# Performance work log

Hardware: AMD Instinct MI355X
Metric: run time of the kernel (lower is better)

Reference implementation:

```python
import jax, jax.numpy as jnp
import numpy as np

N = 50000
E = 600000
D_IN = 128
D_HID = 128
D_OUT = 128


def _glorot(key, shape):
    fan_in, fan_out = shape[0], shape[1]
    lim = float(np.sqrt(6.0 / (fan_in + fan_out)))
    return jax.random.uniform(key, shape, jnp.float32, -lim, lim)


def setup_inputs() -> dict:
    key = jax.random.key(0)
    ks = jax.random.split(key, 10)
    x = jax.random.normal(ks[0], (N, D_IN), jnp.float32)
    edge_index = jax.random.randint(ks[1], (2, E), 0, N, jnp.int64)
    # layer 1 params
    W_pool1 = _glorot(ks[2], (D_IN, D_HID))
    b_pool1 = jnp.zeros((D_HID,), jnp.float32)
    W_upd1 = _glorot(ks[3], (D_IN + D_HID, D_HID))
    b_upd1 = jnp.zeros((D_HID,), jnp.float32)
    # layer 2 params
    W_pool2 = _glorot(ks[4], (D_HID, D_OUT))
    b_pool2 = jnp.zeros((D_OUT,), jnp.float32)
    W_upd2 = _glorot(ks[5], (D_HID + D_OUT, D_OUT))
    b_upd2 = jnp.zeros((D_OUT,), jnp.float32)
    return {
        "x": x, "edge_index": edge_index,
        "W_pool1": W_pool1, "b_pool1": b_pool1, "W_upd1": W_upd1, "b_upd1": b_upd1,
        "W_pool2": W_pool2, "b_pool2": b_pool2, "W_upd2": W_upd2, "b_upd2": b_upd2,
    }


def _pool_sage_conv(x, src, dst, W_pool, b_pool, W_upd, b_upd):
    # message: ReLU(W_pool x_j + b) on gathered source features  [E, out]
    msg = jax.nn.relu(x[src] @ W_pool + b_pool)
    # aggregate: element-wise max over incoming edges per destination node
    agg = jax.ops.segment_max(msg, dst, num_segments=x.shape[0])
    # nodes with no in-edges get -inf from segment_max; torch code zeros non-finite
    agg = jnp.where(jnp.isfinite(agg), agg, jnp.zeros_like(agg))
    # update: ReLU(W_upd [x_v ; h_N(v)] + b)
    out = jax.nn.relu(jnp.concatenate([x, agg], axis=-1) @ W_upd + b_upd)
    return out


def reference(x, edge_index,
              W_pool1, b_pool1, W_upd1, b_upd1,
              W_pool2, b_pool2, W_upd2, b_upd2):
    src, dst = edge_index[0], edge_index[1]
    h = _pool_sage_conv(x, src, dst, W_pool1, b_pool1, W_upd1, b_upd1)
    h = _pool_sage_conv(h, src, dst, W_pool2, b_pool2, W_upd2, b_upd2)
    return h
```

## Files before the change

kernel.cpp:

```cpp
#include <hip/hip_runtime.h>

#define D 128
#define SLOTS 64
#define SLOTP 66
#define NBUCK 800
#define BSLOT 1024
#define EPB 8192

typedef __attribute__((ext_vector_type(8))) short bf16x8;
typedef __attribute__((ext_vector_type(4))) float f32x4;
typedef __attribute__((ext_vector_type(8))) unsigned short u16x8;

__device__ __forceinline__ unsigned short f2bf(float f) {
    unsigned u = __float_as_uint(f);
    u = u + 0x7fffu + ((u >> 16) & 1u);
    return (unsigned short)(u >> 16);
}

__device__ __forceinline__ void pack_one(const float* __restrict__ W,
                                         unsigned short* __restrict__ out, int g, int l) {
    const int kt = g >> 3, nt = g & 7;
    u16x8 pv;
#pragma unroll
    for (int j = 0; j < 8; ++j)
        pv[j] = f2bf(W[(size_t)(kt * 32 + (l >> 4) * 8 + j) * D + nt * 16 + (l & 15)]);
    *(u16x8*)&out[((size_t)g * 64 + l) * 8] = pv;
}

__global__ void prep_kernel(const float4* __restrict__ x4, ushort4* __restrict__ xb4, int n4,
                            const float* __restrict__ Wp1, const float* __restrict__ Wu1,
                            const float* __restrict__ Wp2, const float* __restrict__ Wu2,
                            unsigned short* __restrict__ Wp1p, unsigned short* __restrict__ Wu1p,
                            unsigned short* __restrict__ Wp2p, unsigned short* __restrict__ Wu2p,
                            const int* __restrict__ src, const int* __restrict__ dst,
                            int* __restrict__ gcur, int* __restrict__ bebuf, int E,
                            int EB1, int CB) {
    int b = blockIdx.x;
    const int t = threadIdx.x;
    if (b < EB1) {
        __shared__ int hist[NBUCK];
        __shared__ int boff[NBUCK];
        for (int i = t; i < NBUCK; i += 256) hist[i] = 0;
        __syncthreads();
        const int4* dst4 = (const int4*)dst;
        const int4* src4 = (const int4*)src;
        const int q0 = b * (EPB / 4);
        const int nq = (E + 3) / 4;
#pragma unroll
        for (int k = 0; k < EPB / 4; k += 256) {
            int qi = q0 + k + t;
            if (qi < nq) {
                int4 d4 = dst4[qi];
                int e = qi * 4;
                if (e + 0 < E) atomicAdd(&hist[d4.x >> 6], 1);
                if (e + 1 < E) atomicAdd(&hist[d4.y >> 6], 1);
                if (e + 2 < E) atomicAdd(&hist[d4.z >> 6], 1);
                if (e + 3 < E) atomicAdd(&hist[d4.w >> 6], 1);
            }
        }
        __syncthreads();
        for (int i = t; i < NBUCK; i += 256) {
            int c = hist[i];
            boff[i] = c ? atomicAdd(&gcur[i], c) : 0;
            hist[i] = 0;
        }
        __syncthreads();
#pragma unroll
        for (int k = 0; k < EPB / 4; k += 256) {
            int qi = q0 + k + t;
            if (qi < nq) {
                int4 d4 = dst4[qi];
                int4 s4 = src4[qi];
                int e = qi * 4;
#pragma unroll
                for (int j = 0; j < 4; ++j) {
                    int dd = (j == 0) ? d4.x : (j == 1) ? d4.y : (j == 2) ? d4.z : d4.w;
                    int ss = (j == 0) ? s4.x : (j == 1) ? s4.y : (j == 2) ? s4.z : s4.w;
                    if (e + j < E) {
                        int bk = dd >> 6;
                        int r = atomicAdd(&hist[bk], 1);
                        int pos = boff[bk] + r;
                        if (pos < BSLOT)
                            bebuf[(size_t)bk * BSLOT + pos] = (ss & 0xFFFF) | ((dd & 63) << 16);
                    }
                }
            }
        }
        return;
    }
    b -= EB1;
    if (b < CB) {
        int i = b * 256 + t;
        if (i < n4) {
            float4 v = x4[i];
            ushort4 o;
            o.x = f2bf(v.x); o.y = f2bf(v.y); o.z = f2bf(v.z); o.w = f2bf(v.w);
            xb4[i] = o;
        }
        return;
    }
    b -= CB;
    {
        int g = b * 4 + (t >> 6);
        int l = t & 63;
        if (g < 32)       pack_one(Wp1, Wp1p, g, l);
        else if (g < 96)  pack_one(Wu1, Wu1p, g - 32, l);
        else if (g < 128) pack_one(Wp2, Wp2p, g - 96, l);
        else if (g < 192) pack_one(Wu2, Wu2p, g - 128, l);
    }
}

__launch_bounds__(256)
__global__ void pool_mfma(const unsigned short* __restrict__ X0,
                          const unsigned short* __restrict__ Wp,
                          const float* __restrict__ bias,
                          unsigned short* __restrict__ OUT, int n) {
    __shared__ unsigned short tlds[4][16 * D];
    const int t = threadIdx.x, w = t >> 6, l = t & 63;
    const int lrow = l & 15, lk = l >> 4;
    const int r0 = blockIdx.x * 64 + w * 16;
    int arow = r0 + lrow;
    if (arow > n - 1) arow = n - 1;

    f32x4 acc[8];
#pragma unroll
    for (int nt = 0; nt < 8; ++nt) {
        float bv = bias[nt * 16 + lrow];
        acc[nt] = (f32x4){bv, bv, bv, bv};
    }
#pragma unroll
    for (int kt = 0; kt < 4; ++kt) {
        bf16x8 a = *(const bf16x8*)(X0 + (size_t)arow * D + kt * 32 + lk * 8);
#pragma unroll
        for (int nt = 0; nt < 8; ++nt) {
            bf16x8 b = *(const bf16x8*)(Wp + (((size_t)kt * 8 + nt) * 64 + l) * 8);
            acc[nt] = __builtin_amdgcn_mfma_f32_16x16x32_bf16(a, b, acc[nt], 0, 0, 0);
        }
    }
    unsigned short* tt = tlds[w];
#pragma unroll
    for (int nt = 0; nt < 8; ++nt)
#pragma unroll
        for (int r = 0; r < 4; ++r)
            tt[(lk * 4 + r) * D + nt * 16 + lrow] = f2bf(fmaxf(acc[nt][r], 0.f));
    __syncthreads();
#pragma unroll
    for (int p = 0; p < 4; ++p) {
        int flat = p * 512 + l * 8;
        int rt = flat >> 7, col = flat & (D - 1);
        int grow = r0 + rt;
        if (grow < n)
            *(u16x8*)(OUT + (size_t)grow * D + col) = *(const u16x8*)(tt + flat);
    }
}

__device__ __forceinline__ void build_lists(const int* __restrict__ gcur,
                                            const int* __restrict__ bebuf,
                                            int* h2_s, unsigned short* slots_s,
                                            int bid, int t) {
    if (t < 64) h2_s[t] = 0;
    __syncthreads();
    int cnt = gcur[bid];
    if (cnt > BSLOT) cnt = BSLOT;
    const int* bb = bebuf + (size_t)bid * BSLOT;
    for (int i = t; i < cnt; i += 256) {
        int pk = bb[i];
        int nl = pk >> 16;
        int r = atomicAdd(&h2_s[nl], 1);
        if (r < SLOTS) slots_s[nl * SLOTP + r] = (unsigned short)(pk & 0xFFFF);
    }
    __syncthreads();
}

__device__ __forceinline__ void agg_to_lds(const int* h2_s, const unsigned short* slots_s,
                                           const u16x8* __restrict__ P8,
                                           unsigned short* A_s, int n, int t, int base) {
    const int nl = t >> 2;
    const int q = t & 3;
    const int gn = base + nl;
    u16x8 m0[4], m1[4];
#pragma unroll
    for (int c = 0; c < 4; ++c) { m0[c] = (u16x8){0,0,0,0,0,0,0,0}; m1[c] = m0[c]; }
    if (gn < n) {
        int d = h2_s[nl];
        if (d > SLOTS) d = SLOTS;
        const unsigned short* sp = slots_s + nl * SLOTP;
        int j = 0;
        for (; j + 1 < d; j += 2) {
            const u16x8* pa = P8 + (size_t)sp[j] * 16 + q * 4;
            const u16x8* pb = P8 + (size_t)sp[j + 1] * 16 + q * 4;
            u16x8 a0 = pa[0], a1 = pa[1], a2 = pa[2], a3 = pa[3];
            u16x8 b0 = pb[0], b1 = pb[1], b2 = pb[2], b3 = pb[3];
            m0[0] = __builtin_elementwise_max(m0[0], a0);
            m0[1] = __builtin_elementwise_max(m0[1], a1);
            m0[2] = __builtin_elementwise_max(m0[2], a2);
            m0[3] = __builtin_elementwise_max(m0[3], a3);
            m1[0] = __builtin_elementwise_max(m1[0], b0);
            m1[1] = __builtin_elementwise_max(m1[1], b1);
            m1[2] = __builtin_elementwise_max(m1[2], b2);
            m1[3] = __builtin_elementwise_max(m1[3], b3);
        }
        if (j < d) {
            const u16x8* pa = P8 + (size_t)sp[j] * 16 + q * 4;
#pragma unroll
            for (int c = 0; c < 4; ++c) m0[c] = __builtin_elementwise_max(m0[c], pa[c]);
        }
#pragma unroll
        for (int c = 0; c < 4; ++c) m0[c] = __builtin_elementwise_max(m0[c], m1[c]);
    }
#pragma unroll
    for (int c = 0; c < 4; ++c) {
        int col = q * 32 + c * 8;
        *(u16x8*)&A_s[nl * D + (col ^ ((nl & 7) << 3))] = m0[c];
    }
}

__device__ __forceinline__ bf16x8 lds_afrag(const unsigned short* S, int row, int kbase) {
    return *(const bf16x8*)&S[row * D + (kbase ^ ((row & 7) << 3))];
}

__launch_bounds__(256)
__global__ void fused_upd_pool(const unsigned short* __restrict__ xb,
                               const u16x8* __restrict__ Pb8,
                               const unsigned short* __restrict__ Wu1p, const float* __restrict__ bu1,
                               const unsigned short* __restrict__ Wp2p, const float* __restrict__ bp2,
                               const int* __restrict__ gcur, const int* __restrict__ bebuf,
                               unsigned short* __restrict__ Hb, unsigned short* __restrict__ P2b,
                               int n) {
    __shared__ unsigned short A_s[64 * D];
    __shared__ unsigned short H_s[64 * D];
    __shared__ unsigned short slots_s[64 * SLOTP];
    __shared__ int h2_s[64];
    const int t = threadIdx.x, w = t >> 6, l = t & 63;
    const int base = blockIdx.x * 64;
    const int lrow = l & 15, lk = l >> 4;

    const int r0 = base + w * 16;
    int arow = r0 + lrow;
    if (arow > n - 1) arow = n - 1;

    bf16x8 a_pre[4];
#pragma unroll
    for (int kt = 0; kt < 4; ++kt)
        a_pre[kt] = *(const bf16x8*)(xb + (size_t)arow * D + kt * 32 + lk * 8);

    build_lists(gcur, bebuf, h2_s, slots_s, blockIdx.x, t);
    agg_to_lds(h2_s, slots_s, Pb8, A_s, n, t, base);
    __syncthreads();

    f32x4 acc[8];
#pragma unroll
    for (int nt = 0; nt < 8; ++nt) {
        float bv = bu1[nt * 16 + lrow];
        acc[nt] = (f32x4){bv, bv, bv, bv};
    }
#pragma unroll
    for (int kt = 0; kt < 4; ++kt) {
#pragma unroll
        for (int nt = 0; nt < 8; ++nt) {
            bf16x8 b = *(const bf16x8*)(Wu1p + (((size_t)kt * 8 + nt) * 64 + l) * 8);
            acc[nt] = __builtin_amdgcn_mfma_f32_16x16x32_bf16(a_pre[kt], b, acc[nt], 0, 0, 0);
        }
    }
#pragma unroll
    for (int kt = 4; kt < 8; ++kt) {
        bf16x8 a = lds_afrag(A_s, w * 16 + lrow, (kt - 4) * 32 + lk * 8);
#pragma unroll
        for (int nt = 0; nt < 8; ++nt) {
            bf16x8 b = *(const bf16x8*)(Wu1p + (((size_t)kt * 8 + nt) * 64 + l) * 8);
            acc[nt] = __builtin_amdgcn_mfma_f32_16x16x32_bf16(a, b, acc[nt], 0, 0, 0);
        }
    }

#pragma unroll
    for (int nt = 0; nt < 8; ++nt)
#pragma unroll
        for (int r = 0; r < 4; ++r) {
            int row = w * 16 + lk * 4 + r;
            int col = nt * 16 + lrow;
            H_s[row * D + (col ^ ((row & 7) << 3))] = f2bf(fmaxf(acc[nt][r], 0.f));
        }
    __syncthreads();

#pragma unroll
    for (int p = 0; p < 4; ++p) {
        int flat = p * 512 + l * 8;
        int rt = flat >> 7, col = flat & (D - 1);
        int grow = r0 + rt;
        if (grow < n)
            *(u16x8*)(Hb + (size_t)grow * D + col) =
                *(const u16x8*)&H_s[(w * 16 + rt) * D + (col ^ ((rt & 7) << 3))];
    }

    f32x4 acc2[8];
#pragma unroll
    for (int nt = 0; nt < 8; ++nt) {
        float bv = bp2[nt * 16 + lrow];
        acc2[nt] = (f32x4){bv, bv, bv, bv};
    }
#pragma unroll
    for (int kt = 0; kt < 4; ++kt) {
        bf16x8 a = lds_afrag(H_s, w * 16 + lrow, kt * 32 + lk * 8);
#pragma unroll
        for (int nt = 0; nt < 8; ++nt) {
            bf16x8 b = *(const bf16x8*)(Wp2p + (((size_t)kt * 8 + nt) * 64 + l) * 8);
            acc2[nt] = __builtin_amdgcn_mfma_f32_16x16x32_bf16(a, b, acc2[nt], 0, 0, 0);
        }
    }
    unsigned short* tt = A_s + w * 16 * D;
#pragma unroll
    for (int nt = 0; nt < 8; ++nt)
#pragma unroll
        for (int r = 0; r < 4; ++r)
            tt[(lk * 4 + r) * D + nt * 16 + lrow] = f2bf(fmaxf(acc2[nt][r], 0.f));
    __syncthreads();
#pragma unroll
    for (int p = 0; p < 4; ++p) {
        int flat = p * 512 + l * 8;
        int rt = flat >> 7, col = flat & (D - 1);
        int grow = r0 + rt;
        if (grow < n)
            *(u16x8*)(P2b + (size_t)grow * D + col) = *(const u16x8*)(tt + flat);
    }
}

__launch_bounds__(256)
__global__ void fused_upd2(const unsigned short* __restrict__ Hb,
                           const u16x8* __restrict__ P2b8,
                           const unsigned short* __restrict__ Wu2p, const float* __restrict__ bu2,
                           const int* __restrict__ gcur, const int* __restrict__ bebuf,
                           float* __restrict__ out, int n) {
    __shared__ __align__(16) unsigned char smem[64 * D * 4];
    __shared__ unsigned short slots_s[64 * SLOTP];
    __shared__ int h2_s[64];
    unsigned short* A_s = (unsigned short*)smem;
    float* T_s = (float*)smem;
    const int t = threadIdx.x, w = t >> 6, l = t & 63;
    const int base = blockIdx.x * 64;
    const int lrow = l & 15, lk = l >> 4;

    const int r0 = base + w * 16;
    int arow = r0 + lrow;
    if (arow > n - 1) arow = n - 1;

    bf16x8 a_pre[4];
#pragma unroll
    for (int kt = 0; kt < 4; ++kt)
        a_pre[kt] = *(const bf16x8*)(Hb + (size_t)arow * D + kt * 32 + lk * 8);

    build_lists(gcur, bebuf, h2_s, slots_s, blockIdx.x, t);
    agg_to_lds(h2_s, slots_s, P2b8, A_s, n, t, base);
    __syncthreads();

    f32x4 acc[8];
#pragma unroll
    for (int nt = 0; nt < 8; ++nt) {
        float bv = bu2[nt * 16 + lrow];
        acc[nt] = (f32x4){bv, bv, bv, bv};
    }
#pragma unroll
    for (int kt = 0; kt < 4; ++kt) {
#pragma unroll
        for (int nt = 0; nt < 8; ++nt) {
            bf16x8 b = *(const bf16x8*)(Wu2p + (((size_t)kt * 8 + nt) * 64 + l) * 8);
            acc[nt] = __builtin_amdgcn_mfma_f32_16x16x32_bf16(a_pre[kt], b, acc[nt], 0, 0, 0);
        }
    }
#pragma unroll
    for (int kt = 4; kt < 8; ++kt) {
        bf16x8 a = lds_afrag(A_s, w * 16 + lrow, (kt - 4) * 32 + lk * 8);
#pragma unroll
        for (int nt = 0; nt < 8; ++nt) {
            bf16x8 b = *(const bf16x8*)(Wu2p + (((size_t)kt * 8 + nt) * 64 + l) * 8);
            acc[nt] = __builtin_amdgcn_mfma_f32_16x16x32_bf16(a, b, acc[nt], 0, 0, 0);
        }
    }
    __syncthreads();

    float* tt = T_s + w * 16 * D;
#pragma unroll
    for (int nt = 0; nt < 8; ++nt)
#pragma unroll
        for (int r = 0; r < 4; ++r)
            tt[(lk * 4 + r) * D + nt * 16 + lrow] = fmaxf(acc[nt][r], 0.f);
    __syncthreads();
#pragma unroll
    for (int p = 0; p < 8; ++p) {
        int flat = p * 256 + l * 4;
        int rt = flat >> 7, col = flat & (D - 1);
        int grow = r0 + rt;
        if (grow < n)
            *(float4*)(out + (size_t)grow * D + col) = *(const float4*)(tt + flat);
    }
}

extern "C" void kernel_launch(void* const* d_in, const int* in_sizes, int n_in,
                              void* d_out, int out_size, void* d_ws, size_t ws_size,
                              hipStream_t stream) {
    const float* x   = (const float*)d_in[0];
    const int*   ei  = (const int*)d_in[1];
    const float* Wp1 = (const float*)d_in[2];
    const float* bp1 = (const float*)d_in[3];
    const float* Wu1 = (const float*)d_in[4];
    const float* bu1 = (const float*)d_in[5];
    const float* Wp2 = (const float*)d_in[6];
    const float* bp2 = (const float*)d_in[7];
    const float* Wu2 = (const float*)d_in[8];
    const float* bu2 = (const float*)d_in[9];
    float* out = (float*)d_out;

    const int n = in_sizes[0] / D;
    const int E = in_sizes[1] / 2;
    const int* src = ei;
    const int* dst = ei + E;

    unsigned short* xb   = (unsigned short*)d_ws;
    unsigned short* Pb   = xb + (size_t)n * D;
    unsigned short* Hb   = Pb + (size_t)n * D;
    unsigned short* P2b  = Hb + (size_t)n * D;
    unsigned short* Wp1p = P2b + (size_t)n * D;
    unsigned short* Wu1p = Wp1p + D * D;
    unsigned short* Wp2p = Wu1p + 2 * D * D;
    unsigned short* Wu2p = Wp2p + D * D;
    int* gcur  = (int*)(Wu2p + 2 * D * D);
    int* bebuf = gcur + NBUCK;

    const int gb  = (n + 63) / 64;
    const int CB  = (n * D / 4 + 255) / 256;
    const int PB  = 48;
    const int EB1 = (E + EPB - 1) / EPB;

    hipMemsetAsync(gcur, 0, NBUCK * sizeof(int), stream);
    prep_kernel<<<EB1 + CB + PB, 256, 0, stream>>>(
        (const float4*)x, (ushort4*)xb, n * D / 4,
        Wp1, Wu1, Wp2, Wu2, Wp1p, Wu1p, Wp2p, Wu2p, src, dst, gcur, bebuf, E, EB1, CB);

    pool_mfma<<<gb, 256, 0, stream>>>(xb, Wp1p, bp1, Pb, n);
    fused_upd_pool<<<gb, 256, 0, stream>>>(xb, (const u16x8*)Pb, Wu1p, bu1, Wp2p, bp2,
                                           gcur, bebuf, Hb, P2b, n);
    fused_upd2<<<gb, 256, 0, stream>>>(Hb, (const u16x8*)P2b, Wu2p, bu2,
                                       gcur, bebuf, out, n);
}
```

Before: 116.5 us.

## Sub-bucket edges by source octant so gathers across blocks hit common L2 region

Edges are now binned by destination 64-node block and additionally by the source-index octant (src>>13), giving 8 sub-buckets per block. The aggregation walks the octants in lockstep with a block-wide sync after each, so all blocks tend to gather from the same 8K-node slice of the message table at once. The aim is better cache locality for the random gathers. In exchange it adds an LDS histogram of 6400 entries in the prep kernel, 8 extra barriers per block, and per-octant caps (16 slots per node per octant, 224 per sub-bucket) that could drop edges for high in-degree nodes.

Result: slower. 145.0 us (+24.4%).

```diff
diff --git a/kernel.cpp b/kernel.cpp
--- a/kernel.cpp
+++ b/kernel.cpp
@@ -1,10 +1,11 @@
 #include <hip/hip_runtime.h>
 
 #define D 128
-#define SLOTS 64
-#define SLOTP 66
-#define NBUCK 800
-#define BSLOT 1024
+#define NOCT 8
+#define CSLOT 16
+#define SLOTP 132
+#define NSUB 6400
+#define BSLOT 224
 #define EPB 8192
 
 typedef __attribute__((ext_vector_type(8))) short bf16x8;
@@ -38,46 +39,45 @@
     int b = blockIdx.x;
     const int t = threadIdx.x;
     if (b < EB1) {
-        __shared__ int hist[NBUCK];
-        __shared__ int boff[NBUCK];
-        for (int i = t; i < NBUCK; i += 256) hist[i] = 0;
+        __shared__ int hist[NSUB];
+        __shared__ int boff[NSUB];
+        for (int i = t; i < NSUB; i += 256) hist[i] = 0;
         __syncthreads();
         const int4* dst4 = (const int4*)dst;
         const int4* src4 = (const int4*)src;
         const int q0 = b * (EPB / 4);
         const int nq = (E + 3) / 4;
-#pragma unroll
-        for (int k = 0; k < EPB / 4; k += 256) {
-            int qi = q0 + k + t;
-            if (qi < nq) {
-                int4 d4 = dst4[qi];
-                int e = qi * 4;
-                if (e + 0 < E) atomicAdd(&hist[d4.x >> 6], 1);
-                if (e + 1 < E) atomicAdd(&hist[d4.y >> 6], 1);
-                if (e + 2 < E) atomicAdd(&hist[d4.z >> 6], 1);
-                if (e + 3 < E) atomicAdd(&hist[d4.w >> 6], 1);
-            }
-        }
-        __syncthreads();
-        for (int i = t; i < NBUCK; i += 256) {
-            int c = hist[i];
-            boff[i] = c ? atomicAdd(&gcur[i], c) : 0;
-            hist[i] = 0;
-        }
-        __syncthreads();
-#pragma unroll
         for (int k = 0; k < EPB / 4; k += 256) {
             int qi = q0 + k + t;
             if (qi < nq) {
                 int4 d4 = dst4[qi];
                 int4 s4 = src4[qi];
                 int e = qi * 4;
+                if (e + 0 < E) atomicAdd(&hist[((d4.x >> 6) << 3) | ((s4.x >> 13) & 7)], 1);
+                if (e + 1 < E) atomicAdd(&hist[((d4.y >> 6) << 3) | ((s4.y >> 13) & 7)], 1);
+                if (e + 2 < E) atomicAdd(&hist[((d4.z >> 6) << 3) | ((s4.z >> 13) & 7)], 1);
+                if (e + 3 < E) atomicAdd(&hist[((d4.w >> 6) << 3) | ((s4.w >> 13) & 7)], 1);
+            }
+        }
+        __syncthreads();
+        for (int i = t; i < NSUB; i += 256) {
+            int c = hist[i];
+            boff[i] = c ? atomicAdd(&gcur[i], c) : 0;
+            hist[i] = 0;
+        }
+        __syncthreads();
+        for (int k = 0; k < EPB / 4; k += 256) {
+            int qi = q0 + k + t;
+            if (qi < nq) {
+                int4 d4 = dst4[qi];
+                int4 s4 = src4[qi];
+                int e = qi * 4;
 #pragma unroll
                 for (int j = 0; j < 4; ++j) {
                     int dd = (j == 0) ? d4.x : (j == 1) ? d4.y : (j == 2) ? d4.z : d4.w;
                     int ss = (j == 0) ? s4.x : (j == 1) ? s4.y : (j == 2) ? s4.z : s4.w;
                     if (e + j < E) {
-                        int bk = dd >> 6;
+                        int bk = ((dd >> 6) << 3) | ((ss >> 13) & 7);
                         int r = atomicAdd(&hist[bk], 1);
                         int pos = boff[bk] + r;
                         if (pos < BSLOT)
@@ -154,60 +154,64 @@
     }
 }
 
-__device__ __forceinline__ void build_lists(const int* __restrict__ gcur,
-                                            const int* __restrict__ bebuf,
-                                            int* h2_s, unsigned short* slots_s,
-                                            int bid, int t) {
-    if (t < 64) h2_s[t] = 0;
-    __syncthreads();
-    int cnt = gcur[bid];
-    if (cnt > BSLOT) cnt = BSLOT;
-    const int* bb = bebuf + (size_t)bid * BSLOT;
-    for (int i = t; i < cnt; i += 256) {
-        int pk = bb[i];
-        int nl = pk >> 16;
-        int r = atomicAdd(&h2_s[nl], 1);
-        if (r < SLOTS) slots_s[nl * SLOTP + r] = (unsigned short)(pk & 0xFFFF);
-    }
-    __syncthreads();
-}
-
-__device__ __forceinline__ void agg_to_lds(const int* h2_s, const unsigned short* slots_s,
-                                           const u16x8* __restrict__ P8,
-                                           unsigned short* A_s, int n, int t, int base) {
-    const int nl = t >> 2;
-    const int q = t & 3;
+__device__ __forceinline__ void build_agg(const int* __restrict__ gcur,
+                                          const int* __restrict__ bebuf,
+                                          int* cnt_s, unsigned short* slots_s, int* sub_cnt,
+                                          const u16x8* __restrict__ P8,
+                                          unsigned short* A_s,
+                                          int n, int t, int base, int bid) {
+    if (t < NOCT) {
+        int c = gcur[bid * NOCT + t];
+        sub_cnt[t] = (c > BSLOT) ? BSLOT : c;
+    }
+    for (int i = t; i < 64 * NOCT; i += 256) cnt_s[i] = 0;
+    __syncthreads();
+    for (int i = t; i < NOCT * BSLOT; i += 256) {
+        int oct = i / BSLOT, idx = i - oct * BSLOT;
+        if (idx < sub_cnt[oct]) {
+            int pk = bebuf[((size_t)bid * NOCT + oct) * BSLOT + idx];
+            int nl = pk >> 16;
+            int r = atomicAdd(&cnt_s[nl * NOCT + oct], 1);
+            if (r < CSLOT) slots_s[nl * SLOTP + oct * CSLOT + r] = (unsigned short)(pk & 0xFFFF);
+        }
+    }
+    __syncthreads();
+
+    const int nl = t >> 2, q = t & 3;
     const int gn = base + nl;
     u16x8 m0[4], m1[4];
 #pragma unroll
     for (int c = 0; c < 4; ++c) { m0[c] = (u16x8){0,0,0,0,0,0,0,0}; m1[c] = m0[c]; }
-    if (gn < n) {
-        int d = h2_s[nl];
-        if (d > SLOTS) d = SLOTS;
-        const unsigned short* sp = slots_s + nl * SLOTP;
-        int j = 0;
-        for (; j + 1 < d; j += 2) {
-            const u16x8* pa = P8 + (size_t)sp[j] * 16 + q * 4;
-            const u16x8* pb = P8 + (size_t)sp[j + 1] * 16 + q * 4;
-            u16x8 a0 = pa[0], a1 = pa[1], a2 = pa[2], a3 = pa[3];
-            u16x8 b0 = pb[0], b1 = pb[1], b2 = pb[2], b3 = pb[3];
-            m0[0] = __builtin_elementwise_max(m0[0], a0);
-            m0[1] = __builtin_elementwise_max(m0[1], a1);
-            m0[2] = __builtin_elementwise_max(m0[2], a2);
-            m0[3] = __builtin_elementwise_max(m0[3], a3);
-            m1[0] = __builtin_elementwise_max(m1[0], b0);
-            m1[1] = __builtin_elementwise_max(m1[1], b1);
-            m1[2] = __builtin_elementwise_max(m1[2], b2);
-            m1[3] = __builtin_elementwise_max(m1[3], b3);
-        }
-        if (j < d) {
-            const u16x8* pa = P8 + (size_t)sp[j] * 16 + q * 4;
-#pragma unroll
-            for (int c = 0; c < 4; ++c) m0[c] = __builtin_elementwise_max(m0[c], pa[c]);
-        }
-#pragma unroll
-        for (int c = 0; c < 4; ++c) m0[c] = __builtin_elementwise_max(m0[c], m1[c]);
-    }
+    for (int oct = 0; oct < NOCT; ++oct) {
+        if (gn < n) {
+            int d = cnt_s[nl * NOCT + oct];
+            if (d > CSLOT) d = CSLOT;
+            const unsigned short* sp = slots_s + nl * SLOTP + oct * CSLOT;
+            int j = 0;
+            for (; j + 1 < d; j += 2) {
+                const u16x8* pa = P8 + (size_t)sp[j] * 16 + q * 4;
+                const u16x8* pb = P8 + (size_t)sp[j + 1] * 16 + q * 4;
+                u16x8 a0 = pa[0], a1 = pa[1], a2 = pa[2], a3 = pa[3];
+                u16x8 b0 = pb[0], b1 = pb[1], b2 = pb[2], b3 = pb[3];
+                m0[0] = __builtin_elementwise_max(m0[0], a0);
+                m0[1] = __builtin_elementwise_max(m0[1], a1);
+                m0[2] = __builtin_elementwise_max(m0[2], a2);
+                m0[3] = __builtin_elementwise_max(m0[3], a3);
+                m1[0] = __builtin_elementwise_max(m1[0], b0);
+                m1[1] = __builtin_elementwise_max(m1[1], b1);
+                m1[2] = __builtin_elementwise_max(m1[2], b2);
+                m1[3] = __builtin_elementwise_max(m1[3], b3);
+            }
+            if (j < d) {
+                const u16x8* pa = P8 + (size_t)sp[j] * 16 + q * 4;
+#pragma unroll
+                for (int c = 0; c < 4; ++c) m0[c] = __builtin_elementwise_max(m0[c], pa[c]);
+            }
+        }
+        __syncthreads();
+    }
+#pragma unroll
+    for (int c = 0; c < 4; ++c) m0[c] = __builtin_elementwise_max(m0[c], m1[c]);
 #pragma unroll
     for (int c = 0; c < 4; ++c) {
         int col = q * 32 + c * 8;
@@ -230,7 +234,8 @@
     __shared__ unsigned short A_s[64 * D];
     __shared__ unsigned short H_s[64 * D];
     __shared__ unsigned short slots_s[64 * SLOTP];
-    __shared__ int h2_s[64];
+    __shared__ int cnt_s[64 * NOCT];
+    __shared__ int sub_cnt[NOCT];
     const int t = threadIdx.x, w = t >> 6, l = t & 63;
     const int base = blockIdx.x * 64;
     const int lrow = l & 15, lk = l >> 4;
@@ -244,8 +249,7 @@
     for (int kt = 0; kt < 4; ++kt)
         a_pre[kt] = *(const bf16x8*)(xb + (size_t)arow * D + kt * 32 + lk * 8);
 
-    build_lists(gcur, bebuf, h2_s, slots_s, blockIdx.x, t);
-    agg_to_lds(h2_s, slots_s, Pb8, A_s, n, t, base);
+    build_agg(gcur, bebuf, cnt_s, slots_s, sub_cnt, Pb8, A_s, n, t, base, blockIdx.x);
     __syncthreads();
 
     f32x4 acc[8];
@@ -332,7 +336,8 @@
                            float* __restrict__ out, int n) {
     __shared__ __align__(16) unsigned char smem[64 * D * 4];
     __shared__ unsigned short slots_s[64 * SLOTP];
-    __shared__ int h2_s[64];
+    __shared__ int cnt_s[64 * NOCT];
+    __shared__ int sub_cnt[NOCT];
     unsigned short* A_s = (unsigned short*)smem;
     float* T_s = (float*)smem;
     const int t = threadIdx.x, w = t >> 6, l = t & 63;
@@ -348,8 +353,7 @@
     for (int kt = 0; kt < 4; ++kt)
         a_pre[kt] = *(const bf16x8*)(Hb + (size_t)arow * D + kt * 32 + lk * 8);
 
-    build_lists(gcur, bebuf, h2_s, slots_s, blockIdx.x, t);
-    agg_to_lds(h2_s, slots_s, P2b8, A_s, n, t, base);
+    build_agg(gcur, bebuf, cnt_s, slots_s, sub_cnt, P2b8, A_s, n, t, base, blockIdx.x);
     __syncthreads();
 
     f32x4 acc[8];
@@ -423,14 +427,14 @@
     unsigned short* Wp2p = Wu1p + 2 * D * D;
     unsigned short* Wu2p = Wp2p + D * D;
     int* gcur  = (int*)(Wu2p + 2 * D * D);
-    int* bebuf = gcur + NBUCK;
+    int* bebuf = gcur + NSUB;
 
     const int gb  = (n + 63) / 64;
     const int CB  = (n * D / 4 + 255) / 256;
     const int PB  = 48;
     const int EB1 = (E + EPB - 1) / EPB;
 
-    hipMemsetAsync(gcur, 0, NBUCK * sizeof(int), stream);
+    hipMemsetAsync(gcur, 0, NSUB * sizeof(int), stream);
     prep_kernel<<<EB1 + CB + PB, 256, 0, stream>>>(
         (const float4*)x, (ushort4*)xb, n * D / 4,
         Wp1, Wu1, Wp2, Wu2, Wp1p, Wu1p, Wp2p, Wu2p, src, dst, gcur, bebuf, E, EB1, CB);
```

## Use 512-thread blocks splitting gather and MFMA columns across two wave halves

Applied to the files above, without the earlier changes.

The two fused update kernels now launch 512 threads per 64-node block instead of 256. The max-aggregation gather uses 8 threads per node with 2 vectors each, and the MFMA work is split so each wave covers 4 of the 8 output column tiles. Slot lists and counters are aliased into existing LDS buffers to keep shared memory flat. This aims to raise parallelism and memory-level concurrency in the latency-bound gather, at the cost of duplicated A-fragment loads per wave pair and more block-wide syncs. The old gn<n guard in the aggregation was dropped, so tail rows rely on zero bucket counts.

After: 114.6 us. About the same (-1.7%).

```diff
diff --git a/kernel.cpp b/kernel.cpp
--- a/kernel.cpp
+++ b/kernel.cpp
@@ -154,16 +154,17 @@
     }
 }
 
-__device__ __forceinline__ void build_lists(const int* __restrict__ gcur,
-                                            const int* __restrict__ bebuf,
-                                            int* h2_s, unsigned short* slots_s,
-                                            int bid, int t) {
+
+__device__ __forceinline__ void build_lists512(const int* __restrict__ gcur,
+                                               const int* __restrict__ bebuf,
+                                               int* h2_s, unsigned short* slots_s,
+                                               int bid, int t) {
     if (t < 64) h2_s[t] = 0;
     __syncthreads();
     int cnt = gcur[bid];
     if (cnt > BSLOT) cnt = BSLOT;
     const int* bb = bebuf + (size_t)bid * BSLOT;
-    for (int i = t; i < cnt; i += 256) {
+    for (int i = t; i < cnt; i += 512) {
         int pk = bb[i];
         int nl = pk >> 16;
         int r = atomicAdd(&h2_s[nl], 1);
@@ -172,45 +173,38 @@
     __syncthreads();
 }
 
-__device__ __forceinline__ void agg_to_lds(const int* h2_s, const unsigned short* slots_s,
-                                           const u16x8* __restrict__ P8,
-                                           unsigned short* A_s, int n, int t, int base) {
-    const int nl = t >> 2;
-    const int q = t & 3;
-    const int gn = base + nl;
-    u16x8 m0[4], m1[4];
-#pragma unroll
-    for (int c = 0; c < 4; ++c) { m0[c] = (u16x8){0,0,0,0,0,0,0,0}; m1[c] = m0[c]; }
-    if (gn < n) {
-        int d = h2_s[nl];
-        if (d > SLOTS) d = SLOTS;
-        const unsigned short* sp = slots_s + nl * SLOTP;
-        int j = 0;
-        for (; j + 1 < d; j += 2) {
-            const u16x8* pa = P8 + (size_t)sp[j] * 16 + q * 4;
-            const u16x8* pb = P8 + (size_t)sp[j + 1] * 16 + q * 4;
-            u16x8 a0 = pa[0], a1 = pa[1], a2 = pa[2], a3 = pa[3];
-            u16x8 b0 = pb[0], b1 = pb[1], b2 = pb[2], b3 = pb[3];
-            m0[0] = __builtin_elementwise_max(m0[0], a0);
-            m0[1] = __builtin_elementwise_max(m0[1], a1);
-            m0[2] = __builtin_elementwise_max(m0[2], a2);
-            m0[3] = __builtin_elementwise_max(m0[3], a3);
-            m1[0] = __builtin_elementwise_max(m1[0], b0);
-            m1[1] = __builtin_elementwise_max(m1[1], b1);
-            m1[2] = __builtin_elementwise_max(m1[2], b2);
-            m1[3] = __builtin_elementwise_max(m1[3], b3);
-        }
-        if (j < d) {
-            const u16x8* pa = P8 + (size_t)sp[j] * 16 + q * 4;
-#pragma unroll
-            for (int c = 0; c < 4; ++c) m0[c] = __builtin_elementwise_max(m0[c], pa[c]);
-        }
-#pragma unroll
-        for (int c = 0; c < 4; ++c) m0[c] = __builtin_elementwise_max(m0[c], m1[c]);
-    }
-#pragma unroll
-    for (int c = 0; c < 4; ++c) {
-        int col = q * 32 + c * 8;
+__device__ __forceinline__ void agg512(const int* h2_s, const unsigned short* slots_s,
+                                       const u16x8* __restrict__ P8,
+                                       unsigned short* A_s, int t) {
+    const int nl = t >> 3;
+    const int q = t & 7;
+    u16x8 m0[2], m1[2];
+#pragma unroll
+    for (int c = 0; c < 2; ++c) { m0[c] = (u16x8){0,0,0,0,0,0,0,0}; m1[c] = m0[c]; }
+    int d = h2_s[nl];
+    if (d > SLOTS) d = SLOTS;
+    const unsigned short* sp = slots_s + nl * SLOTP;
+    int j = 0;
+    for (; j + 1 < d; j += 2) {
+        const u16x8* pa = P8 + (size_t)sp[j] * 16 + q * 2;
+        const u16x8* pb = P8 + (size_t)sp[j + 1] * 16 + q * 2;
+        u16x8 a0 = pa[0], a1 = pa[1];
+        u16x8 b0 = pb[0], b1 = pb[1];
+        m0[0] = __builtin_elementwise_max(m0[0], a0);
+        m0[1] = __builtin_elementwise_max(m0[1], a1);
+        m1[0] = __builtin_elementwise_max(m1[0], b0);
+        m1[1] = __builtin_elementwise_max(m1[1], b1);
+    }
+    if (j < d) {
+        const u16x8* pa = P8 + (size_t)sp[j] * 16 + q * 2;
+        m0[0] = __builtin_elementwise_max(m0[0], pa[0]);
+        m0[1] = __builtin_elementwise_max(m0[1], pa[1]);
+    }
+    m0[0] = __builtin_elementwise_max(m0[0], m1[0]);
+    m0[1] = __builtin_elementwise_max(m0[1], m1[1]);
+#pragma unroll
+    for (int c = 0; c < 2; ++c) {
+        int col = q * 16 + c * 8;
         *(u16x8*)&A_s[nl * D + (col ^ ((nl & 7) << 3))] = m0[c];
     }
 }
@@ -219,7 +213,7 @@
     return *(const bf16x8*)&S[row * D + (kbase ^ ((row & 7) << 3))];
 }
 
-__launch_bounds__(256)
+__launch_bounds__(512)
 __global__ void fused_upd_pool(const unsigned short* __restrict__ xb,
                                const u16x8* __restrict__ Pb8,
                                const unsigned short* __restrict__ Wu1p, const float* __restrict__ bu1,
@@ -229,13 +223,14 @@
                                int n) {
     __shared__ unsigned short A_s[64 * D];
     __shared__ unsigned short H_s[64 * D];
-    __shared__ unsigned short slots_s[64 * SLOTP];
-    __shared__ int h2_s[64];
+    unsigned short* slots_s = H_s;
+    int* h2_s = (int*)(H_s + 64 * SLOTP);
     const int t = threadIdx.x, w = t >> 6, l = t & 63;
     const int base = blockIdx.x * 64;
     const int lrow = l & 15, lk = l >> 4;
-
-    const int r0 = base + w * 16;
+    const int s = w & 3, h = w >> 2;
+
+    const int r0 = base + s * 16;
     int arow = r0 + lrow;
     if (arow > n - 1) arow = n - 1;
 
@@ -244,102 +239,106 @@
     for (int kt = 0; kt < 4; ++kt)
         a_pre[kt] = *(const bf16x8*)(xb + (size_t)arow * D + kt * 32 + lk * 8);
 
-    build_lists(gcur, bebuf, h2_s, slots_s, blockIdx.x, t);
-    agg_to_lds(h2_s, slots_s, Pb8, A_s, n, t, base);
-    __syncthreads();
-
-    f32x4 acc[8];
-#pragma unroll
-    for (int nt = 0; nt < 8; ++nt) {
-        float bv = bu1[nt * 16 + lrow];
-        acc[nt] = (f32x4){bv, bv, bv, bv};
+    build_lists512(gcur, bebuf, h2_s, slots_s, blockIdx.x, t);
+    agg512(h2_s, slots_s, Pb8, A_s, t);
+    __syncthreads();
+
+    f32x4 acc[4];
+#pragma unroll
+    for (int ntl = 0; ntl < 4; ++ntl) {
+        float bv = bu1[(h * 4 + ntl) * 16 + lrow];
+        acc[ntl] = (f32x4){bv, bv, bv, bv};
     }
 #pragma unroll
     for (int kt = 0; kt < 4; ++kt) {
 #pragma unroll
-        for (int nt = 0; nt < 8; ++nt) {
-            bf16x8 b = *(const bf16x8*)(Wu1p + (((size_t)kt * 8 + nt) * 64 + l) * 8);
-            acc[nt] = __builtin_amdgcn_mfma_f32_16x16x32_bf16(a_pre[kt], b, acc[nt], 0, 0, 0);
+        for (int ntl = 0; ntl < 4; ++ntl) {
+            bf16x8 b = *(const bf16x8*)(Wu1p + (((size_t)kt * 8 + h * 4 + ntl) * 64 + l) * 8);
+            acc[ntl] = __builtin_amdgcn_mfma_f32_16x16x32_bf16(a_pre[kt], b, acc[ntl], 0, 0, 0);
         }
     }
 #pragma unroll
     for (int kt = 4; kt < 8; ++kt) {
-        bf16x8 a = lds_afrag(A_s, w * 16 + lrow, (kt - 4) * 32 + lk * 8);
-#pragma unroll
-        for (int nt = 0; nt < 8; ++nt) {
-            bf16x8 b = *(const bf16x8*)(Wu1p + (((size_t)kt * 8 + nt) * 64 + l) * 8);
-            acc[nt] = __builtin_amdgcn_mfma_f32_16x16x32_bf16(a, b, acc[nt], 0, 0, 0);
-        }
-    }
-
-#pragma unroll
-    for (int nt = 0; nt < 8; ++nt)
+        bf16x8 a = lds_afrag(A_s, s * 16 + lrow, (kt - 4) * 32 + lk * 8);
+#pragma unroll
+        for (int ntl = 0; ntl < 4; ++ntl) {
+            bf16x8 b = *(const bf16x8*)(Wu1p + (((size_t)kt * 8 + h * 4 + ntl) * 64 + l) * 8);
+            acc[ntl] = __builtin_amdgcn_mfma_f32_16x16x32_bf16(a, b, acc[ntl], 0, 0, 0);
+        }
+    }
+
+#pragma unroll
+    for (int ntl = 0; ntl < 4; ++ntl)
 #pragma unroll
         for (int r = 0; r < 4; ++r) {
-            int row = w * 16 + lk * 4 + r;
-            int col = nt * 16 + lrow;
-            H_s[row * D + (col ^ ((row & 7) << 3))] = f2bf(fmaxf(acc[nt][r], 0.f));
-        }
-    __syncthreads();
-
-#pragma unroll
-    for (int p = 0; p < 4; ++p) {
-        int flat = p * 512 + l * 8;
+            int row = s * 16 + lk * 4 + r;
+            int col = (h * 4 + ntl) * 16 + lrow;
+            H_s[row * D + (col ^ ((row & 7) << 3))] = f2bf(fmaxf(acc[ntl][r], 0.f));
+        }
+    __syncthreads();
+
+#pragma unroll
+    for (int p = 0; p < 2; ++p) {
+        int flat = p * 4096 + t * 8;
         int rt = flat >> 7, col = flat & (D - 1);
-        int grow = r0 + rt;
+        int grow = base + rt;
         if (grow < n)
             *(u16x8*)(Hb + (size_t)grow * D + col) =
-                *(const u16x8*)&H_s[(w * 16 + rt) * D + (col ^ ((rt & 7) << 3))];
-    }
-
-    f32x4 acc2[8];
-#pragma unroll
-    for (int nt = 0; nt < 8; ++nt) {
-        float bv = bp2[nt * 16 + lrow];
-        acc2[nt] = (f32x4){bv, bv, bv, bv};
+                *(const u16x8*)&H_s[rt * D + (col ^ ((rt & 7) << 3))];
+    }
+
+    f32x4 acc2[4];
+#pragma unroll
+    for (int ntl = 0; ntl < 4; ++ntl) {
+        float bv = bp2[(h * 4 + ntl) * 16 + lrow];
+        acc2[ntl] = (f32x4){bv, bv, bv, bv};
     }
 #pragma unroll
     for (int kt = 0; kt < 4; ++kt) {
-        bf16x8 a = lds_afrag(H_s, w * 16 + lrow, kt * 32 + lk * 8);
-#pragma unroll
-        for (int nt = 0; nt < 8; ++nt) {
-            bf16x8 b = *(const bf16x8*)(Wp2p + (((size_t)kt * 8 + nt) * 64 + l) * 8);
-            acc2[nt] = __builtin_amdgcn_mfma_f32_16x16x32_bf16(a, b, acc2[nt], 0, 0, 0);
-        }
-    }
-    unsigned short* tt = A_s + w * 16 * D;
-#pragma unroll
-    for (int nt = 0; nt < 8; ++nt)
-#pragma unroll
-        for (int r = 0; r < 4; ++r)
-            tt[(lk * 4 + r) * D + nt * 16 + lrow] = f2bf(fmaxf(acc2[nt][r], 0.f));
-    __syncthreads();
-#pragma unroll
-    for (int p = 0; p < 4; ++p) {
-        int flat = p * 512 + l * 8;
+        bf16x8 a = lds_afrag(H_s, s * 16 + lrow, kt * 32 + lk * 8);
+#pragma unroll
+        for (int ntl = 0; ntl < 4; ++ntl) {
+            bf16x8 b = *(const bf16x8*)(Wp2p + (((size_t)kt * 8 + h * 4 + ntl) * 64 + l) * 8);
+            acc2[ntl] = __builtin_amdgcn_mfma_f32_16x16x32_bf16(a, b, acc2[ntl], 0, 0, 0);
+        }
+    }
+#pragma unroll
+    for (int ntl = 0; ntl < 4; ++ntl)
+#pragma unroll
+        for (int r = 0; r < 4; ++r) {
+            int row = s * 16 + lk * 4 + r;
+            int col = (h * 4 + ntl) * 16 + lrow;
+            A_s[row * D + (col ^ ((row & 7) << 3))] = f2bf(fmaxf(acc2[ntl][r], 0.f));
+        }
+    __syncthreads();
+#pragma unroll
+    for (int p = 0; p < 2; ++p) {
+        int flat = p * 4096 + t * 8;
         int rt = flat >> 7, col = flat & (D - 1);
-        int grow = r0 + rt;
+        int grow = base + rt;
         if (grow < n)
-            *(u16x8*)(P2b + (size_t)grow * D + col) = *(const u16x8*)(tt + flat);
-    }
-}
-
-__launch_bounds__(256)
+            *(u16x8*)(P2b + (size_t)grow * D + col) =
+                *(const u16x8*)&A_s[rt * D + (col ^ ((rt & 7) << 3))];
+    }
+}
+
+__launch_bounds__(512)
 __global__ void fused_upd2(const unsigned short* __restrict__ Hb,
                            const u16x8* __restrict__ P2b8,
                            const unsigned short* __restrict__ Wu2p, const float* __restrict__ bu2,
                            const int* __restrict__ gcur, const int* __restrict__ bebuf,
                            float* __restrict__ out, int n) {
     __shared__ __align__(16) unsigned char smem[64 * D * 4];
-    __shared__ unsigned short slots_s[64 * SLOTP];
-    __shared__ int h2_s[64];
     unsigned short* A_s = (unsigned short*)smem;
+    unsigned short* slots_s = (unsigned short*)(smem + 64 * D * 2);
+    int* h2_s = (int*)(smem + 64 * D * 2 + 64 * SLOTP * 2);
     float* T_s = (float*)smem;
     const int t = threadIdx.x, w = t >> 6, l = t & 63;
     const int base = blockIdx.x * 64;
     const int lrow = l & 15, lk = l >> 4;
-
-    const int r0 = base + w * 16;
+    const int s = w & 3, h = w >> 2;
+
+    const int r0 = base + s * 16;
     int arow = r0 + lrow;
     if (arow > n - 1) arow = n - 1;
 
@@ -348,49 +347,51 @@
     for (int kt = 0; kt < 4; ++kt)
         a_pre[kt] = *(const bf16x8*)(Hb + (size_t)arow * D + kt * 32 + lk * 8);
 
-    build_lists(gcur, bebuf, h2_s, slots_s, blockIdx.x, t);
-    agg_to_lds(h2_s, slots_s, P2b8, A_s, n, t, base);
-    __syncthreads();
-
-    f32x4 acc[8];
-#pragma unroll
-    for (int nt = 0; nt < 8; ++nt) {
-        float bv = bu2[nt * 16 + lrow];
-        acc[nt] = (f32x4){bv, bv, bv, bv};
+    build_lists512(gcur, bebuf, h2_s, slots_s, blockIdx.x, t);
+    agg512(h2_s, slots_s, P2b8, A_s, t);
+    __syncthreads();
+
+    f32x4 acc[4];
+#pragma unroll
+    for (int ntl = 0; ntl < 4; ++ntl) {
+        float bv = bu2[(h * 4 + ntl) * 16 + lrow];
+        acc[ntl] = (f32x4){bv, bv, bv, bv};
     }
 #pragma unroll
     for (int kt = 0; kt < 4; ++kt) {
 #pragma unroll
-        for (int nt = 0; nt < 8; ++nt) {
-            bf16x8 b = *(const bf16x8*)(Wu2p + (((size_t)kt * 8 + nt) * 64 + l) * 8);
-            acc[nt] = __builtin_amdgcn_mfma_f32_16x16x32_bf16(a_pre[kt], b, acc[nt], 0, 0, 0);
+        for (int ntl = 0; ntl < 4; ++ntl) {
+            bf16x8 b = *(const bf16x8*)(Wu2p + (((size_t)kt * 8 + h * 4 + ntl) * 64 + l) * 8);
+            acc[ntl] = __builtin_amdgcn_mfma_f32_16x16x32_bf16(a_pre[kt], b, acc[ntl], 0, 0, 0);
         }
     }
 #pragma unroll
     for (int kt = 4; kt < 8; ++kt) {
-        bf16x8 a = lds_afrag(A_s, w * 16 + lrow, (kt - 4) * 32 + lk * 8);
-#pragma unroll
-        for (int nt = 0; nt < 8; ++nt) {
-            bf16x8 b = *(const bf16x8*)(Wu2p + (((size_t)kt * 8 + nt) * 64 + l) * 8);
-            acc[nt] = __builtin_amdgcn_mfma_f32_16x16x32_bf16(a, b, acc[nt], 0, 0, 0);
-        }
-    }
-    __syncthreads();
-
-    float* tt = T_s + w * 16 * D;
-#pragma unroll
-    for (int nt = 0; nt < 8; ++nt)
-#pragma unroll
-        for (int r = 0; r < 4; ++r)
-            tt[(lk * 4 + r) * D + nt * 16 + lrow] = fmaxf(acc[nt][r], 0.f);
-    __syncthreads();
-#pragma unroll
-    for (int p = 0; p < 8; ++p) {
-        int flat = p * 256 + l * 4;
+        bf16x8 a = lds_afrag(A_s, s * 16 + lrow, (kt - 4) * 32 + lk * 8);
+#pragma unroll
+        for (int ntl = 0; ntl < 4; ++ntl) {
+            bf16x8 b = *(const bf16x8*)(Wu2p + (((size_t)kt * 8 + h * 4 + ntl) * 64 + l) * 8);
+            acc[ntl] = __builtin_amdgcn_mfma_f32_16x16x32_bf16(a, b, acc[ntl], 0, 0, 0);
+        }
+    }
+    __syncthreads();
+
+#pragma unroll
+    for (int ntl = 0; ntl < 4; ++ntl)
+#pragma unroll
+        for (int r = 0; r < 4; ++r) {
+            int row = s * 16 + lk * 4 + r;
+            int col = (h * 4 + ntl) * 16 + lrow;
+            T_s[row * D + col] = fmaxf(acc[ntl][r], 0.f);
+        }
+    __syncthreads();
+#pragma unroll
+    for (int p = 0; p < 4; ++p) {
+        int flat = p * 2048 + t * 4;
         int rt = flat >> 7, col = flat & (D - 1);
-        int grow = r0 + rt;
+        int grow = base + rt;
         if (grow < n)
-            *(float4*)(out + (size_t)grow * D + col) = *(const float4*)(tt + flat);
+            *(float4*)(out + (size_t)grow * D + col) = *(const float4*)(T_s + flat);
     }
 }
 
@@ -436,8 +437,8 @@
         Wp1, Wu1, Wp2, Wu2, Wp1p, Wu1p, Wp2p, Wu2p, src, dst, gcur, bebuf, E, EB1, CB);
 
     pool_mfma<<<gb, 256, 0, stream>>>(xb, Wp1p, bp1, Pb, n);
-    fused_upd_pool<<<gb, 256, 0, stream>>>(xb, (const u16x8*)Pb, Wu1p, bu1, Wp2p, bp2,
+    fused_upd_pool<<<gb, 512, 0, stream>>>(xb, (const u16x8*)Pb, Wu1p, bu1, Wp2p, bp2,
                                            gcur, bebuf, Hb, P2b, n);
-    fused_upd2<<<gb, 256, 0, stream>>>(Hb, (const u16x8*)P2b, Wu2p, bu2,
+    fused_upd2<<<gb, 512, 0, stream>>>(Hb, (const u16x8*)P2b, Wu2p, bu2,
                                        gcur, bebuf, out, n);
 }
```
